# Kernel optimization log

Hardware: AMD Instinct MI355X
Metric: run time of the kernel (lower is better)

The kernel has to match this reference:

```python
import jax, jax.numpy as jnp
import numpy as np

NUM_CHUNKS = 8
TOP_K = 2
IN_F = 4096
HID_F = 4096
OUT_F = 4096
B = 4096


def setup_inputs() -> dict:
    key = jax.random.key(0)
    k = jax.random.split(key, 5)
    cin = IN_F // NUM_CHUNKS    # 512
    cout = HID_F // NUM_CHUNKS  # 512
    s_in = 1.0 / np.sqrt(cin)
    s_fin = 1.0 / np.sqrt(cout * TOP_K)
    return {
        "x": jax.random.normal(k[0], (B, IN_F), dtype=jnp.float32),
        # stacked chunk-expert Linear params: y = x @ W + b
        "W_chunks": jax.random.uniform(k[1], (NUM_CHUNKS, cin, cout), jnp.float32, -s_in, s_in),
        "b_chunks": jax.random.uniform(k[2], (NUM_CHUNKS, cout), jnp.float32, -s_in, s_in),
        "W_final": jax.random.uniform(k[3], (cout * TOP_K, OUT_F), jnp.float32, -s_fin, s_fin),
        "b_final": jax.random.uniform(k[4], (OUT_F,), jnp.float32, -s_fin, s_fin),
    }


def reference(x, W_chunks, b_chunks, W_final, b_final):
    Bsz = x.shape[0]
    # split into chunks along feature dim: (B, num_chunks, chunk_in)
    xr = x.reshape(Bsz, NUM_CHUNKS, -1)
    # per-chunk activity = mean(|chunk|) over the whole batch (matches torch .abs().mean())
    activities = jnp.mean(jnp.abs(xr), axis=(0, 2))  # (num_chunks,)
    _, topk_idx = jax.lax.top_k(activities, TOP_K)    # descending, like torch.topk
    # gather selected chunks and their expert weights, run small GEMMs
    x_sel = xr[:, topk_idx, :]                        # (B, k, chunk_in)
    h = jnp.einsum('bkc,kcd->bkd', x_sel, W_chunks[topk_idx]) + b_chunks[topk_idx]
    h = h.reshape(Bsz, -1)                            # concat along feature dim
    out = h @ W_final + b_final                       # (B, out_features)
    return out
```

## Files before the change

### kernel.cpp

```cpp
#include <hip/hip_runtime.h>


typedef __bf16 bf16x8_t __attribute__((ext_vector_type(8)));
typedef float  f32x4_t  __attribute__((ext_vector_type(4)));

__device__ inline unsigned short f2bf(float f) {
    __bf16 b = (__bf16)f;
    return __builtin_bit_cast(unsigned short, b);
}

__device__ inline void stage_glds(const unsigned short* gtile, int stride, int row0,
                                  unsigned short* lds, int lane) {
    const int r8 = lane >> 3;
    const int gg = (lane & 7) ^ r8;
    const unsigned short* gp = gtile + (size_t)(row0 + r8) * stride + gg * 8;
    unsigned short* lp = lds + row0 * 64;
    __builtin_amdgcn_global_load_lds((const __attribute__((address_space(1))) void*)gp,
                                     (__attribute__((address_space(3))) void*)lp,
                                     16, 0, 0);
}

__device__ inline bf16x8_t ldsfrag(const unsigned short* Ls, int row, int kb) {
    return *(const bf16x8_t*)(Ls + row * 64 + (((kb >> 3) ^ (row & 7)) * 8));
}

__global__ void fused_prep_kernel(const float* __restrict__ x, const float* __restrict__ Wc,
                                  const float* __restrict__ Wf, float* __restrict__ part,
                                  unsigned short* __restrict__ wct, unsigned short* __restrict__ wft) {
    const int b = blockIdx.x;
    const int tid = threadIdx.x;

    if (b < 512) {
        const int chunk = b & 7;
        const int rg = b >> 3;
        const int colf4 = tid & 127;
        const int rsub = tid >> 7;
        const float4* base = (const float4*)x + (size_t)chunk * 128 + colf4;
        float s = 0.f;
        #pragma unroll 4
        for (int i = 0; i < 32; ++i) {
            int row = rg * 64 + i * 2 + rsub;
            float4 v = base[(size_t)row * 1024];
            s += fabsf(v.x) + fabsf(v.y) + fabsf(v.z) + fabsf(v.w);
        }
        #pragma unroll
        for (int off = 32; off > 0; off >>= 1) s += __shfl_down(s, off, 64);
        __shared__ float wsum[4];
        if ((tid & 63) == 0) wsum[tid >> 6] = s;
        __syncthreads();
        if (tid == 0) part[chunk * 64 + rg] = wsum[0] + wsum[1] + wsum[2] + wsum[3];
        return;
    }

    __shared__ float tile[32][33];
    const int tx = tid & 31, ty = tid >> 5;
    const float* src; unsigned short* dst; int R, C, cb, rb;
    int jj = b - 512;
    if (jj < 4096) {
        src = Wf; dst = wft; R = 1024; C = 4096;
        cb = (jj & 127) * 32; rb = (jj >> 7) * 32;
    } else {
        jj -= 4096;
        int c = jj >> 8, t = jj & 255;
        src = Wc + (size_t)c * 262144;
        dst = wct + (size_t)c * 262144;
        R = 512; C = 512;
        cb = (t & 15) * 32; rb = (t >> 4) * 32;
    }
    #pragma unroll
    for (int i = 0; i < 4; ++i)
        tile[ty + i * 8][tx] = src[(size_t)(rb + ty + i * 8) * C + cb + tx];
    __syncthreads();
    #pragma unroll
    for (int i = 0; i < 4; ++i)
        dst[(size_t)(cb + ty + i * 8) * R + rb + tx] = f2bf(tile[tx][ty + i * 8]);
}

__global__ __launch_bounds__(256, 4)
void gemm1_kernel(const float* __restrict__ x, const unsigned short* __restrict__ wct,
                  const float* __restrict__ bc, const float* __restrict__ part,
                  unsigned short* __restrict__ h) {
    __shared__ __align__(16) unsigned char lds_raw[24576];
    unsigned short* As = (unsigned short*)lds_raw;
    unsigned short* Bs = (unsigned short*)(lds_raw + 8192);

    const int tid = threadIdx.x;
    const int wave = tid >> 6;
    const int lane = tid & 63;

    {
        float* sred = (float*)lds_raw;
        sred[tid] = part[tid];
        sred[tid + 256] = part[tid + 256];
        __syncthreads();
        float* act8 = (float*)(lds_raw + 2048);
        if (tid < 8) {
            float a = 0.f;
            #pragma unroll
            for (int k = 0; k < 64; ++k) a += sred[tid * 64 + k];
            act8[tid] = a;
        }
        __syncthreads();
    }
    int sel0, sel1;
    {
        const float* act8 = (const float*)(lds_raw + 2048);
        float v0 = -1e30f, v1 = -1e30f; int b0 = 0, b1 = 0;
        #pragma unroll
        for (int i = 0; i < 8; ++i) {
            float v = act8[i];
            if (v > v0) { v1 = v0; b1 = b0; v0 = v; b0 = i; }
            else if (v > v1) { v1 = v; b1 = i; }
        }
        sel0 = b0; sel1 = b1;
    }
    __syncthreads();

    const int z = blockIdx.z;
    const int idxz = z ? sel1 : sel0;
    const int m0 = blockIdx.x * 64;
    const int n0 = blockIdx.y * 128;
    const int wm = (wave >> 1) * 32;
    const int wn = (wave & 1) * 64;
    const int rl = lane & 15;
    const int quad = lane >> 4;

    const float* xtile = x + (size_t)m0 * 4096 + idxz * 512;
    const unsigned short* Btile = wct + (size_t)idxz * 262144 + (size_t)n0 * 512;

    f32x4_t acc[2][4] = {};
    const int ar = tid >> 2;
    const int aq = tid & 3;

    for (int k0 = 0; k0 < 512; k0 += 64) {
        #pragma unroll
        for (int s = wave; s < 16; s += 4)
            stage_glds(Btile + k0, 512, s * 8, Bs, lane);
        const float* gr = xtile + (size_t)ar * 4096 + k0;
        #pragma unroll
        for (int j = 0; j < 2; ++j) {
            int gg = aq * 2 + j;
            float4 a = *(const float4*)(gr + gg * 8);
            float4 c = *(const float4*)(gr + gg * 8 + 4);
            bf16x8_t v;
            v[0] = (__bf16)a.x; v[1] = (__bf16)a.y; v[2] = (__bf16)a.z; v[3] = (__bf16)a.w;
            v[4] = (__bf16)c.x; v[5] = (__bf16)c.y; v[6] = (__bf16)c.z; v[7] = (__bf16)c.w;
            *(bf16x8_t*)(As + ar * 64 + ((gg ^ (ar & 7)) * 8)) = v;
        }
        __syncthreads();
        #pragma unroll
        for (int kq = 0; kq < 2; ++kq) {
            const int kb = kq * 32 + quad * 8;
            bf16x8_t af[2], bfr[4];
            #pragma unroll
            for (int i = 0; i < 2; ++i) af[i]  = ldsfrag(As, wm + i * 16 + rl, kb);
            #pragma unroll
            for (int i = 0; i < 4; ++i) bfr[i] = ldsfrag(Bs, wn + i * 16 + rl, kb);
            #pragma unroll
            for (int mi = 0; mi < 2; ++mi)
                #pragma unroll
                for (int ni = 0; ni < 4; ++ni)
                    acc[mi][ni] = __builtin_amdgcn_mfma_f32_16x16x32_bf16(af[mi], bfr[ni], acc[mi][ni], 0, 0, 0);
        }
        __syncthreads();
    }

    const int row_l = quad * 4;
    const float* bias = bc + (size_t)idxz * 512;
    #pragma unroll
    for (int ni = 0; ni < 4; ++ni) {
        int col = n0 + wn + ni * 16 + rl;
        float bv = bias[col];
        #pragma unroll
        for (int mi = 0; mi < 2; ++mi) {
            #pragma unroll
            for (int j = 0; j < 4; ++j) {
                int row = m0 + wm + mi * 16 + row_l + j;
                h[(size_t)row * 1024 + z * 512 + col] = f2bf(acc[mi][ni][j] + bv);
            }
        }
    }
}

__global__ __launch_bounds__(256, 4)
void gemm2_kernel(const unsigned short* __restrict__ h, const unsigned short* __restrict__ wft,
                  const float* __restrict__ bfin, float* __restrict__ out) {
    __shared__ __align__(16) unsigned short As[128 * 64];
    __shared__ __align__(16) unsigned short Bs[128 * 64];
    const int m0 = blockIdx.x * 128;
    const int n0 = blockIdx.y * 128;
    const int tid = threadIdx.x;
    const int wave = tid >> 6;
    const int lane = tid & 63;
    const int wm = (wave >> 1) * 64;
    const int wn = (wave & 1) * 64;
    const int rl = lane & 15;
    const int quad = lane >> 4;

    const unsigned short* Atile = h + (size_t)m0 * 1024;
    const unsigned short* Btile = wft + (size_t)n0 * 1024;

    f32x4_t acc[4][4] = {};

    for (int k0 = 0; k0 < 1024; k0 += 64) {
        #pragma unroll
        for (int s = wave; s < 32; s += 4) {
            if (s < 16) stage_glds(Atile + k0, 1024, s * 8, As, lane);
            else        stage_glds(Btile + k0, 1024, (s - 16) * 8, Bs, lane);
        }
        __syncthreads();
        #pragma unroll
        for (int kq = 0; kq < 2; ++kq) {
            const int kb = kq * 32 + quad * 8;
            bf16x8_t af[4], bfr[4];
            #pragma unroll
            for (int i = 0; i < 4; ++i) {
                af[i]  = ldsfrag(As, wm + i * 16 + rl, kb);
                bfr[i] = ldsfrag(Bs, wn + i * 16 + rl, kb);
            }
            #pragma unroll
            for (int mi = 0; mi < 4; ++mi)
                #pragma unroll
                for (int ni = 0; ni < 4; ++ni)
                    acc[mi][ni] = __builtin_amdgcn_mfma_f32_16x16x32_bf16(af[mi], bfr[ni], acc[mi][ni], 0, 0, 0);
        }
        __syncthreads();
    }

    const int row_l = quad * 4;
    float bv[4];
    #pragma unroll
    for (int ni = 0; ni < 4; ++ni) bv[ni] = bfin[n0 + wn + ni * 16 + rl];
    #pragma unroll
    for (int j = 0; j < 4; ++j) {
        #pragma unroll
        for (int mi = 0; mi < 4; ++mi) {
            int row = m0 + wm + mi * 16 + row_l + j;
            float* orow = out + (size_t)row * 4096 + n0 + wn + rl;
            #pragma unroll
            for (int ni = 0; ni < 4; ++ni)
                orow[ni * 16] = acc[mi][ni][j] + bv[ni];
        }
    }
}

extern "C" void kernel_launch(void* const* d_in, const int* in_sizes, int n_in,
                              void* d_out, int out_size, void* d_ws, size_t ws_size,
                              hipStream_t stream) {
    const float* x    = (const float*)d_in[0];
    const float* Wc   = (const float*)d_in[1];
    const float* bc   = (const float*)d_in[2];
    const float* Wf   = (const float*)d_in[3];
    const float* bfin = (const float*)d_in[4];
    float* out = (float*)d_out;

    float* part = (float*)d_ws;
    unsigned short* h   = (unsigned short*)((char*)d_ws + 4096);
    unsigned short* wct = h   + (size_t)4096 * 1024;
    unsigned short* wft = wct + (size_t)8 * 512 * 512;

    fused_prep_kernel<<<6656, 256, 0, stream>>>(x, Wc, Wf, part, wct, wft);
    gemm1_kernel<<<dim3(64, 4, 2), 256, 0, stream>>>(x, wct, bc, part, h);
    gemm2_kernel<<<dim3(32, 32, 1), 256, 0, stream>>>(h, wft, bfin, out);
}
```

Baseline: 183.2 us.

## Rewrite gemm2 as 256x256 tile with 4-stage async LDS pipeline

The second GEMM moves from 128x128 tiles with 256 threads and a synchronous K=64 loop to 256x256 tiles with 512 threads. It adds a 4-buffer pipeline of direct global-to-LDS loads over K=32 slices, with explicit vmcnt waits, a single barrier per step, and raised priority around the MFMA block. The aim is to hide global load latency and raise arithmetic intensity per LDS byte. In exchange it uses 128KB of LDS and more accumulator registers per thread, and launches only 256 blocks, which reduces occupancy and may leave CUs unevenly loaded.

```diff
diff --git a/kernel.cpp b/kernel.cpp
--- a/kernel.cpp
+++ b/kernel.cpp
@@ -22,6 +22,21 @@
 
 __device__ inline bf16x8_t ldsfrag(const unsigned short* Ls, int row, int kb) {
     return *(const bf16x8_t*)(Ls + row * 64 + (((kb >> 3) ^ (row & 7)) * 8));
+}
+
+__device__ inline void stage32(const unsigned short* gtile, int row0,
+                               unsigned short* lds, int lane) {
+    const int r  = lane >> 2;
+    const int gg = (lane & 3) ^ ((r >> 1) & 3);
+    const unsigned short* gp = gtile + (size_t)(row0 + r) * 1024 + gg * 8;
+    unsigned short* lp = lds + row0 * 32;
+    __builtin_amdgcn_global_load_lds((const __attribute__((address_space(1))) void*)gp,
+                                     (__attribute__((address_space(3))) void*)lp,
+                                     16, 0, 0);
+}
+
+__device__ inline bf16x8_t ldsfrag32(const unsigned short* Ls, int row, int kb) {
+    return *(const bf16x8_t*)(Ls + row * 32 + ((((kb >> 3) ^ ((row >> 1) & 3))) * 8));
 }
 
 __global__ void fused_prep_kernel(const float* __restrict__ x, const float* __restrict__ Wc,
@@ -182,61 +197,85 @@
     }
 }
 
-__global__ __launch_bounds__(256, 4)
+__global__ __launch_bounds__(512, 2)
 void gemm2_kernel(const unsigned short* __restrict__ h, const unsigned short* __restrict__ wft,
                   const float* __restrict__ bfin, float* __restrict__ out) {
-    __shared__ __align__(16) unsigned short As[128 * 64];
-    __shared__ __align__(16) unsigned short Bs[128 * 64];
-    const int m0 = blockIdx.x * 128;
-    const int n0 = blockIdx.y * 128;
-    const int tid = threadIdx.x;
-    const int wave = tid >> 6;
+    __shared__ __align__(16) unsigned short lds[65536];
+
+    const int tid  = threadIdx.x;
+    const int wv   = tid >> 6;
     const int lane = tid & 63;
-    const int wm = (wave >> 1) * 64;
-    const int wn = (wave & 1) * 64;
-    const int rl = lane & 15;
+    const int m0 = blockIdx.x * 256;
+    const int n0 = blockIdx.y * 256;
+    const int wmo = (wv >> 2) * 128;
+    const int wno = (wv & 3) * 64;
+    const int rl   = lane & 15;
     const int quad = lane >> 4;
-
-    const unsigned short* Atile = h + (size_t)m0 * 1024;
+    const int kb   = quad * 8;
+    const int srow = wv * 32;
+
+    const unsigned short* Atile = h   + (size_t)m0 * 1024;
     const unsigned short* Btile = wft + (size_t)n0 * 1024;
 
-    f32x4_t acc[4][4] = {};
-
-    for (int k0 = 0; k0 < 1024; k0 += 64) {
-        #pragma unroll
-        for (int s = wave; s < 32; s += 4) {
-            if (s < 16) stage_glds(Atile + k0, 1024, s * 8, As, lane);
-            else        stage_glds(Btile + k0, 1024, (s - 16) * 8, Bs, lane);
-        }
-        __syncthreads();
-        #pragma unroll
-        for (int kq = 0; kq < 2; ++kq) {
-            const int kb = kq * 32 + quad * 8;
-            bf16x8_t af[4], bfr[4];
-            #pragma unroll
-            for (int i = 0; i < 4; ++i) {
-                af[i]  = ldsfrag(As, wm + i * 16 + rl, kb);
-                bfr[i] = ldsfrag(Bs, wn + i * 16 + rl, kb);
-            }
-            #pragma unroll
-            for (int mi = 0; mi < 4; ++mi)
-                #pragma unroll
-                for (int ni = 0; ni < 4; ++ni)
-                    acc[mi][ni] = __builtin_amdgcn_mfma_f32_16x16x32_bf16(af[mi], bfr[ni], acc[mi][ni], 0, 0, 0);
-        }
-        __syncthreads();
-    }
+    f32x4_t acc[8][4] = {};
+
+    #pragma unroll
+    for (int p = 0; p < 3; ++p) {
+        unsigned short* As_n = lds + p * 16384;
+        unsigned short* Bs_n = As_n + 8192;
+        stage32(Atile + p * 32, srow,      As_n, lane);
+        stage32(Atile + p * 32, srow + 16, As_n, lane);
+        stage32(Btile + p * 32, srow,      Bs_n, lane);
+        stage32(Btile + p * 32, srow + 16, Bs_n, lane);
+    }
+
+    #pragma unroll 4
+    for (int t = 0; t < 32; ++t) {
+        __builtin_amdgcn_sched_barrier(0);
+        {
+            const int tn = (t + 3 < 32) ? (t + 3) : 31;
+            unsigned short* As_n = lds + ((t + 3) & 3) * 16384;
+            unsigned short* Bs_n = As_n + 8192;
+            stage32(Atile + tn * 32, srow,      As_n, lane);
+            stage32(Atile + tn * 32, srow + 16, As_n, lane);
+            stage32(Btile + tn * 32, srow,      Bs_n, lane);
+            stage32(Btile + tn * 32, srow + 16, Bs_n, lane);
+        }
+        asm volatile("s_waitcnt vmcnt(12)" ::: "memory");
+        __builtin_amdgcn_sched_barrier(0);
+        __builtin_amdgcn_s_barrier();
+        __builtin_amdgcn_sched_barrier(0);
+
+        const unsigned short* As = lds + (t & 3) * 16384;
+        const unsigned short* Bs = As + 8192;
+        bf16x8_t bfr[4], af[8];
+        #pragma unroll
+        for (int i = 0; i < 4; ++i) bfr[i] = ldsfrag32(Bs, wno + i * 16 + rl, kb);
+        #pragma unroll
+        for (int i = 0; i < 8; ++i) af[i]  = ldsfrag32(As, wmo + i * 16 + rl, kb);
+
+        __builtin_amdgcn_s_setprio(1);
+        #pragma unroll
+        for (int mi = 0; mi < 8; ++mi)
+            #pragma unroll
+            for (int ni = 0; ni < 4; ++ni)
+                acc[mi][ni] = __builtin_amdgcn_mfma_f32_16x16x32_bf16(af[mi], bfr[ni], acc[mi][ni], 0, 0, 0);
+        __builtin_amdgcn_s_setprio(0);
+        __builtin_amdgcn_sched_barrier(0);
+        __builtin_amdgcn_s_barrier();
+    }
+    asm volatile("s_waitcnt vmcnt(0)" ::: "memory");
 
     const int row_l = quad * 4;
     float bv[4];
     #pragma unroll
-    for (int ni = 0; ni < 4; ++ni) bv[ni] = bfin[n0 + wn + ni * 16 + rl];
+    for (int ni = 0; ni < 4; ++ni) bv[ni] = bfin[n0 + wno + ni * 16 + rl];
     #pragma unroll
     for (int j = 0; j < 4; ++j) {
         #pragma unroll
-        for (int mi = 0; mi < 4; ++mi) {
-            int row = m0 + wm + mi * 16 + row_l + j;
-            float* orow = out + (size_t)row * 4096 + n0 + wn + rl;
+        for (int mi = 0; mi < 8; ++mi) {
+            int row = m0 + wmo + mi * 16 + row_l + j;
+            float* orow = out + (size_t)row * 4096 + n0 + wno + rl;
             #pragma unroll
             for (int ni = 0; ni < 4; ++ni)
                 orow[ni * 16] = acc[mi][ni][j] + bv[ni];
@@ -261,5 +300,5 @@
 
     fused_prep_kernel<<<6656, 256, 0, stream>>>(x, Wc, Wf, part, wct, wft);
     gemm1_kernel<<<dim3(64, 4, 2), 256, 0, stream>>>(x, wct, bc, part, h);
-    gemm2_kernel<<<dim3(32, 32, 1), 256, 0, stream>>>(h, wft, bfin, out);
-}
+    gemm2_kernel<<<dim3(16, 16, 1), 512, 0, stream>>>(h, wft, bfin, out);
+}
```

Measured after the change: 184.4 us. About the same (+0.7%).
